# Performance work log

Measured on AMD Instinct MI355X. Metric: run time of the kernel, lower is better.

The kernel has to match this reference:

```python
import jax, jax.numpy as jnp
import numpy as np

TAU = 0.5
EPS = 1e-8


def setup_inputs() -> dict:
    key = jax.random.key(0)
    k1, k2 = jax.random.split(key)
    N, D = 200000, 512
    z_pos = jax.random.normal(k1, (N, D), dtype=jnp.float32)
    W = jax.random.normal(k2, (D, D), dtype=jnp.float32) * (1.0 / np.sqrt(D))
    b = jnp.zeros((D,), dtype=jnp.float32)
    return {"z_pos": z_pos, "W": W, "b": b}


def reference(z_pos, W, b):
    # sample_centroid: softmax-weighted centroid (computed on detached embeddings)
    h = jax.lax.stop_gradient(z_pos)
    init_c = h.mean(axis=0)                              # [D]
    d2 = jnp.sum((h - init_c[None, :]) ** 2, axis=1)     # [N]
    w = jax.nn.softmax(-d2 / TAU)                        # [N]
    c = jnp.sum(h * w[:, None], axis=0)                  # [D]

    # SimNet: dist = 1 - cosine_similarity(proj(x), c)
    x_proj = z_pos @ W.T + b                             # [N, D]
    x_norm = jnp.maximum(jnp.linalg.norm(x_proj, axis=-1), EPS)  # [N]
    c_norm = jnp.maximum(jnp.linalg.norm(c), EPS)
    cos = (x_proj @ c) / (x_norm * c_norm)               # [N]
    dist = 1.0 - cos
    return dist
```

## Files before the change

### kernel.cpp

```cpp
#include <hip/hip_runtime.h>
#include <hip/hip_bf16.h>
#include <math.h>

#define DD 512
#define EPSF 1e-8f
#define BM 128
#define BN 128
#define BK 32
#define FBIG 3.402823466e+38f
#define NPART 2048

typedef __bf16 bf16_t;
typedef __bf16 bf16x4_t __attribute__((ext_vector_type(4)));
typedef __bf16 bf16x8_t __attribute__((ext_vector_type(8)));
typedef float f32x4 __attribute__((ext_vector_type(4)));

__device__ inline float bf2f(unsigned short u) {
    return __uint_as_float(((unsigned int)u) << 16);
}

__global__ void k_convW(const float* __restrict__ W, bf16_t* __restrict__ Wb) {
    int i = blockIdx.x * blockDim.x + threadIdx.x;
    float4 v = ((const float4*)W)[i];
    bf16x4_t o;
    o[0] = (bf16_t)v.x; o[1] = (bf16_t)v.y; o[2] = (bf16_t)v.z; o[3] = (bf16_t)v.w;
    ((bf16x4_t*)Wb)[i] = o;
}

template<bool CONV>
__global__ void k_colsum(const float* __restrict__ z, bf16_t* __restrict__ zb,
                         float* __restrict__ part, int N, int rpb) {
    int t = threadIdx.x;
    int b = blockIdx.x;
    int col4 = t & 127, sub = t >> 7;
    int r0 = b * rpb, r1 = min(r0 + rpb, N);
    const float4* z4 = (const float4*)z;
    float4 acc = make_float4(0.f, 0.f, 0.f, 0.f);
    #pragma unroll 4
    for (int r = r0 + sub; r < r1; r += 2) {
        float4 v = z4[(size_t)r * 128 + col4];
        if (CONV) {
            bf16x4_t o;
            o[0] = (bf16_t)v.x; o[1] = (bf16_t)v.y; o[2] = (bf16_t)v.z; o[3] = (bf16_t)v.w;
            ((bf16x4_t*)zb)[(size_t)r * 128 + col4] = o;
        }
        acc.x += v.x; acc.y += v.y; acc.z += v.z; acc.w += v.w;
    }
    __shared__ float4 sm[128];
    if (sub == 1) sm[col4] = acc;
    __syncthreads();
    if (sub == 0) {
        float4 o = sm[col4];
        acc.x += o.x; acc.y += o.y; acc.z += o.z; acc.w += o.w;
        ((float4*)(part + (size_t)b * DD))[col4] = acc;
    }
}

__global__ void k_reduceP(const float* __restrict__ part, float* __restrict__ outv, float scale) {
    __shared__ float sm[256];
    int j = blockIdx.x;
    int t = threadIdx.x;
    float s = 0.f;
    #pragma unroll
    for (int p = 0; p < NPART / 256; ++p) s += part[(size_t)(p * 256 + t) * DD + j];
    sm[t] = s;
    __syncthreads();
    for (int st = 128; st > 0; st >>= 1) {
        if (t < st) sm[t] += sm[t + st];
        __syncthreads();
    }
    if (t == 0) outv[j] = sm[0] * scale;
}

__global__ __launch_bounds__(256, 4) void k_d2w(
    const float* __restrict__ z, const float* __restrict__ cbar,
    float* __restrict__ part, float* __restrict__ mpart,
    float* __restrict__ spart, int N)
{
    __shared__ float4 cs[128];
    __shared__ float4 vsm[4][128];
    __shared__ float wm[4], wsv[4];
    int t = threadIdx.x;
    int lane = t & 63, wv = t >> 6;
    int l15 = lane & 15, r4 = lane >> 4;
    if (t < 128) cs[t] = ((const float4*)cbar)[t];
    __syncthreads();

    int gw = (blockIdx.x * 256 + t) >> 6;
    int nw = (gridDim.x * 256) >> 6;
    float m = FBIG, s = 0.f;
    float4 acc[8];
    #pragma unroll
    for (int q = 0; q < 8; ++q) acc[q] = make_float4(0.f, 0.f, 0.f, 0.f);

    for (int r = gw * 4 + r4; r < N; r += nw * 4) {
        const float4* zr = (const float4*)(z + (size_t)r * DD);
        float4 vv[8];
        float sum = 0.f;
        #pragma unroll
        for (int q = 0; q < 8; ++q) {
            float4 v = zr[q * 16 + l15];
            float4 c = cs[q * 16 + l15];
            vv[q] = v;
            float d;
            d = v.x - c.x; sum += d * d;
            d = v.y - c.y; sum += d * d;
            d = v.z - c.z; sum += d * d;
            d = v.w - c.w; sum += d * d;
        }
        #pragma unroll
        for (int off = 1; off < 16; off <<= 1) sum += __shfl_xor(sum, off, 64);
        float w;
        if (sum < m) {
            float f = __expf(-2.0f * (m - sum));
            s *= f;
            #pragma unroll
            for (int q = 0; q < 8; ++q) {
                acc[q].x *= f; acc[q].y *= f; acc[q].z *= f; acc[q].w *= f;
            }
            m = sum;
            w = 1.0f;
        } else {
            w = __expf(-2.0f * (sum - m));
        }
        s += w;
        #pragma unroll
        for (int q = 0; q < 8; ++q) {
            acc[q].x += w * vv[q].x; acc[q].y += w * vv[q].y;
            acc[q].z += w * vv[q].z; acc[q].w += w * vv[q].w;
        }
    }

    float mw = fminf(m, __shfl_xor(m, 16, 64));
    mw = fminf(mw, __shfl_xor(mw, 32, 64));
    float f = __expf(-2.0f * (m - mw));
    s *= f;
    #pragma unroll
    for (int q = 0; q < 8; ++q) {
        acc[q].x *= f; acc[q].y *= f; acc[q].z *= f; acc[q].w *= f;
    }
    #pragma unroll
    for (int off = 16; off < 64; off <<= 1) {
        s += __shfl_xor(s, off, 64);
        #pragma unroll
        for (int q = 0; q < 8; ++q) {
            acc[q].x += __shfl_xor(acc[q].x, off, 64);
            acc[q].y += __shfl_xor(acc[q].y, off, 64);
            acc[q].z += __shfl_xor(acc[q].z, off, 64);
            acc[q].w += __shfl_xor(acc[q].w, off, 64);
        }
    }
    if (lane < 16) {
        #pragma unroll
        for (int q = 0; q < 8; ++q) vsm[wv][q * 16 + l15] = acc[q];
        if (lane == 0) { wm[wv] = mw; wsv[wv] = s; }
    }
    __syncthreads();
    if (t < 128) {
        float M = fminf(fminf(wm[0], wm[1]), fminf(wm[2], wm[3]));
        float4 o = make_float4(0.f, 0.f, 0.f, 0.f);
        #pragma unroll
        for (int w2 = 0; w2 < 4; ++w2) {
            float fw = __expf(-2.0f * (wm[w2] - M));
            float4 a = vsm[w2][t];
            o.x += fw * a.x; o.y += fw * a.y; o.z += fw * a.z; o.w += fw * a.w;
        }
        ((float4*)(part + (size_t)blockIdx.x * DD))[t] = o;
        if (t == 0) {
            float S = 0.f;
            #pragma unroll
            for (int w2 = 0; w2 < 4; ++w2) S += wsv[w2] * __expf(-2.0f * (wm[w2] - M));
            mpart[blockIdx.x] = M;
            spart[blockIdx.x] = S;
        }
    }
}

__global__ void k_combine2(const float* __restrict__ mpart, const float* __restrict__ spart,
                           float* __restrict__ wscale) {
    __shared__ float smm[256], sms[256];
    int t = threadIdx.x;
    float M = FBIG;
    for (int i = t; i < NPART; i += 256) M = fminf(M, mpart[i]);
    smm[t] = M;
    __syncthreads();
    for (int st = 128; st > 0; st >>= 1) {
        if (t < st) smm[t] = fminf(smm[t], smm[t + st]);
        __syncthreads();
    }
    M = smm[0];
    float S = 0.f;
    for (int i = t; i < NPART; i += 256) S += spart[i] * __expf(-2.0f * (mpart[i] - M));
    sms[t] = S;
    __syncthreads();
    for (int st = 128; st > 0; st >>= 1) {
        if (t < st) sms[t] += sms[t + st];
        __syncthreads();
    }
    float inv = 1.0f / sms[0];
    for (int i = t; i < NPART; i += 256) wscale[i] = __expf(-2.0f * (mpart[i] - M)) * inv;
}

__global__ void k_reducePW(const float* __restrict__ part, const float* __restrict__ wscale,
                           float* __restrict__ outv) {
    __shared__ float sm[256];
    int j = blockIdx.x, t = threadIdx.x;
    float s = 0.f;
    #pragma unroll
    for (int p = 0; p < NPART / 256; ++p) {
        int b = p * 256 + t;
        s += part[(size_t)b * DD + j] * wscale[b];
    }
    sm[t] = s;
    __syncthreads();
    for (int st = 128; st > 0; st >>= 1) {
        if (t < st) sm[t] += sm[t + st];
        __syncthreads();
    }
    if (t == 0) outv[j] = sm[0];
}

__global__ void k_cnorm(const float* __restrict__ cvec, float* __restrict__ outp) {
    __shared__ float sm[512];
    float v = cvec[threadIdx.x];
    sm[threadIdx.x] = v * v;
    __syncthreads();
    for (int st = 256; st > 0; st >>= 1) {
        if (threadIdx.x < st) sm[threadIdx.x] += sm[threadIdx.x + st];
        __syncthreads();
    }
    if (threadIdx.x == 0) outp[0] = 1.0f / fmaxf(sqrtf(sm[0]), EPSF);
}

__global__ __launch_bounds__(512, 2) void k_gemm256(
    const bf16_t* __restrict__ zb, const bf16_t* __restrict__ Wb,
    const float* __restrict__ bvec, const float* __restrict__ cvec,
    float* __restrict__ sqp, float* __restrict__ dtp, int N, int npad)
{
    __shared__ bf16_t As[2 * 256 * 64];
    __shared__ bf16_t Bs[2 * 256 * 64];

    const int t    = threadIdx.x;
    const int lane = t & 63;
    const int wid  = t >> 6;
    const int wr   = wid >> 2;
    const int wc   = wid & 3;
    const int quad = lane >> 4;
    const int l15  = lane & 15;

    const int nwg = gridDim.x * gridDim.y;
    const int lid = blockIdx.y * gridDim.x + blockIdx.x;
    const int q8  = nwg >> 3, r8 = nwg & 7;
    const int xcd = lid & 7, idx = lid >> 3;
    const int wg  = (xcd < r8 ? xcd * (q8 + 1) : r8 * (q8 + 1) + (xcd - r8) * q8) + idx;
    const int cb     = wg & 1;
    const int row0   = (wg >> 1) * 256;

    const int tr = t >> 3;
    const int bo = ((t & 7) * 16) ^ ((tr & 7) << 4);
    const char* apt = (const char*)zb + (size_t)(row0 + tr) * (DD * 2) + bo;
    const char* bpt = (const char*)Wb + (size_t)(cb * 256 + tr) * (DD * 2) + bo;
    const int ldsw = __builtin_amdgcn_readfirstlane(wid * 1024);

#define STAGE256(buf, kt) do {                                                              \
    _Pragma("unroll")                                                                       \
    for (int r_ = 0; r_ < 4; ++r_) {                                                        \
        __builtin_amdgcn_global_load_lds(                                                   \
            (const __attribute__((address_space(1))) unsigned int*)(const void*)            \
                (apt + (size_t)r_ * 65536 + (kt) * 128),                                    \
            (__attribute__((address_space(3))) unsigned int*)(void*)                        \
                ((char*)As + (buf) * 32768 + r_ * 8192 + ldsw), 16, 0, 0);                  \
        __builtin_amdgcn_global_load_lds(                                                   \
            (const __attribute__((address_space(1))) unsigned int*)(const void*)            \
                (bpt + (size_t)r_ * 65536 + (kt) * 128),                                    \
            (__attribute__((address_space(3))) unsigned int*)(void*)                        \
                ((char*)Bs + (buf) * 32768 + r_ * 8192 + ldsw), 16, 0, 0);                  \
    }                                                                                       \
} while (0)

    const int ka0 = (quad * 16) ^ ((l15 & 7) << 4);
    const int ka1 = ka0 ^ 64;
    const char* abase = (const char*)As + (wr * 128 + l15) * 128;
    const char* bbase = (const char*)Bs + (wc * 64 + l15) * 128;

    f32x4 acc[8][4];
    #pragma unroll
    for (int m = 0; m < 8; ++m)
        #pragma unroll
        for (int n = 0; n < 4; ++n) acc[m][n] = (f32x4){0.f, 0.f, 0.f, 0.f};

    STAGE256(0, 0);
    STAGE256(1, 1);
    asm volatile("s_waitcnt vmcnt(8)" ::: "memory");
    __builtin_amdgcn_sched_barrier(0);
    __builtin_amdgcn_s_barrier();
    __builtin_amdgcn_sched_barrier(0);

    #pragma unroll
    for (int kt = 0; kt < 8; ++kt) {
        const int cur = kt & 1;
        bf16x8_t afr[8][2], bfr[4][2];
        #pragma unroll
        for (int m = 0; m < 8; ++m) {
            afr[m][0] = *(const bf16x8_t*)(abase + cur * 32768 + m * 2048 + ka0);
            afr[m][1] = *(const bf16x8_t*)(abase + cur * 32768 + m * 2048 + ka1);
        }
        #pragma unroll
        for (int n = 0; n < 4; ++n) {
            bfr[n][0] = *(const bf16x8_t*)(bbase + cur * 32768 + n * 2048 + ka0);
            bfr[n][1] = *(const bf16x8_t*)(bbase + cur * 32768 + n * 2048 + ka1);
        }
        asm volatile("s_waitcnt lgkmcnt(0)" ::: "memory");
        __builtin_amdgcn_sched_barrier(0);
        __builtin_amdgcn_s_barrier();
        __builtin_amdgcn_sched_barrier(0);
        if (kt < 6) STAGE256(cur, kt + 2);
        __builtin_amdgcn_sched_barrier(0);
        __builtin_amdgcn_s_setprio(1);
        #pragma unroll
        for (int s = 0; s < 2; ++s)
            #pragma unroll
            for (int m = 0; m < 8; ++m)
                #pragma unroll
                for (int n = 0; n < 4; ++n)
                    acc[m][n] = __builtin_amdgcn_mfma_f32_16x16x32_bf16(
                        afr[m][s], bfr[n][s], acc[m][n], 0, 0, 0);
        __builtin_amdgcn_s_setprio(0);
        if (kt < 6) { asm volatile("s_waitcnt vmcnt(8)" ::: "memory"); }
        else        { asm volatile("s_waitcnt vmcnt(0)" ::: "memory"); }
        __builtin_amdgcn_sched_barrier(0);
        __builtin_amdgcn_s_barrier();
        __builtin_amdgcn_sched_barrier(0);
    }
#undef STAGE256

    float* psq = (float*)As;
    float* pdt = (float*)((char*)As + 16384);
    float bc[4], cc[4];
    #pragma unroll
    for (int n = 0; n < 4; ++n) {
        int col = cb * 256 + wc * 64 + n * 16 + l15;
        bc[n] = bvec[col];
        cc[n] = cvec[col];
    }
    #pragma unroll
    for (int m = 0; m < 8; ++m) {
        #pragma unroll
        for (int rg = 0; rg < 4; ++rg) {
            float sq = 0.f, dt = 0.f;
            #pragma unroll
            for (int n = 0; n < 4; ++n) {
                float x = acc[m][n][rg] + bc[n];
                sq += x * x;
                dt += x * cc[n];
            }
            sq += __shfl_xor(sq, 1, 64); dt += __shfl_xor(dt, 1, 64);
            sq += __shfl_xor(sq, 2, 64); dt += __shfl_xor(dt, 2, 64);
            if ((l15 & 3) == 0) {
                int row = wr * 128 + m * 16 + quad * 4 + rg;
                int slot = wc * 4 + (l15 >> 2);
                psq[row * 16 + slot] = sq;
                pdt[row * 16 + slot] = dt;
            }
        }
    }
    __syncthreads();
    if (t < 256) {
        int r = row0 + t;
        if (r < N) {
            const float4* p4 = (const float4*)(psq + t * 16);
            const float4* d4 = (const float4*)(pdt + t * 16);
            float sq = 0.f, dt = 0.f;
            #pragma unroll
            for (int i = 0; i < 4; ++i) {
                float4 a = p4[i], b2 = d4[i];
                sq += a.x + a.y + a.z + a.w;
                dt += b2.x + b2.y + b2.z + b2.w;
            }
            sqp[(size_t)cb * npad + r] = sq;
            dtp[(size_t)cb * npad + r] = dt;
        }
    }
}

__global__ __launch_bounds__(256, 4) void k_gemm_fb(
    const float* __restrict__ z, const bf16_t* __restrict__ Wb,
    const float* __restrict__ bvec, const float* __restrict__ cvec,
    float* __restrict__ sqp, float* __restrict__ dtp, int N, int npad)
{
    __shared__ bf16_t Asl[BM * BK];
    __shared__ bf16_t Bsl[BN * BK];
    __shared__ float psq[BM][8];
    __shared__ float pdt[BM][8];

    const int t    = threadIdx.x;
    const int lane = t & 63;
    const int wv   = t >> 6;
    const int wrr  = wv >> 1;
    const int wcc  = wv & 1;
    const int quad = lane >> 4;
    const int l15  = lane & 15;
    const int cbx  = blockIdx.x;
    const int row0 = blockIdx.y * BM;

    const bf16_t* bp = Wb + (size_t)(cbx * BN + (t >> 2)) * DD + (t & 3) * 8;
    const int arow = t >> 1;
    const int ah   = t & 1;
    int rowe = row0 + arow; if (rowe >= N) rowe = N - 1;
    const float4* zp4 = (const float4*)(z + (size_t)rowe * DD + ah * 16);

    f32x4 acc[4][4];
    #pragma unroll
    for (int a = 0; a < 4; ++a)
        #pragma unroll
        for (int b = 0; b < 4; ++b) acc[a][b] = (f32x4){0.f, 0.f, 0.f, 0.f};

    float4 v0 = zp4[0], v1 = zp4[1], v2 = zp4[2], v3 = zp4[3];

    for (int kc = 0; kc < DD; kc += BK) {
        if (kc) __syncthreads();
        #pragma unroll
        for (int q = 0; q < 2; ++q) {
            int ldsoff = __builtin_amdgcn_readfirstlane(q * 4096 + wv * 1024);
            __builtin_amdgcn_global_load_lds(
                (const __attribute__((address_space(1))) unsigned int*)(const void*)(bp + (size_t)q * 64 * DD + kc),
                (__attribute__((address_space(3))) unsigned int*)(void*)((char*)Bsl + ldsoff),
                16, 0, 0);
        }
        bf16x8_t lo, hi;
        lo[0]=(bf16_t)v0.x; lo[1]=(bf16_t)v0.y; lo[2]=(bf16_t)v0.z; lo[3]=(bf16_t)v0.w;
        lo[4]=(bf16_t)v1.x; lo[5]=(bf16_t)v1.y; lo[6]=(bf16_t)v1.z; lo[7]=(bf16_t)v1.w;
        hi[0]=(bf16_t)v2.x; hi[1]=(bf16_t)v2.y; hi[2]=(bf16_t)v2.z; hi[3]=(bf16_t)v2.w;
        hi[4]=(bf16_t)v3.x; hi[5]=(bf16_t)v3.y; hi[6]=(bf16_t)v3.z; hi[7]=(bf16_t)v3.w;
        *(bf16x8_t*)(Asl + arow * BK + ah * 16)     = lo;
        *(bf16x8_t*)(Asl + arow * BK + ah * 16 + 8) = hi;
        __syncthreads();
        if (kc + BK < DD) {
            int kf = (kc + BK) >> 2;
            v0 = zp4[kf]; v1 = zp4[kf + 1]; v2 = zp4[kf + 2]; v3 = zp4[kf + 3];
        }
        bf16x8_t af[4];
        #pragma unroll
        for (int rt = 0; rt < 4; ++rt)
            af[rt] = *(const bf16x8_t*)(Asl + (wrr * 64 + rt * 16 + l15) * BK + quad * 8);
        #pragma unroll
        for (int ct = 0; ct < 4; ++ct) {
            bf16x8_t bfv = *(const bf16x8_t*)(Bsl + (wcc * 64 + ct * 16 + l15) * BK + quad * 8);
            #pragma unroll
            for (int rt = 0; rt < 4; ++rt)
                acc[rt][ct] = __builtin_amdgcn_mfma_f32_16x16x32_bf16(af[rt], bfv, acc[rt][ct], 0, 0, 0);
        }
    }

    float bc[4], cc[4];
    #pragma unroll
    for (int ct = 0; ct < 4; ++ct) {
        int col = cbx * BN + wcc * 64 + ct * 16 + l15;
        bc[ct] = bvec[col];
        cc[ct] = cvec[col];
    }
    #pragma unroll
    for (int rt = 0; rt < 4; ++rt) {
        #pragma unroll
        for (int rg = 0; rg < 4; ++rg) {
            float sq = 0.f, dt = 0.f;
            #pragma unroll
            for (int ct = 0; ct < 4; ++ct) {
                float x = acc[rt][ct][rg] + bc[ct];
                sq += x * x;
                dt += x * cc[ct];
            }
            sq += __shfl_xor(sq, 1, 64); dt += __shfl_xor(dt, 1, 64);
            sq += __shfl_xor(sq, 2, 64); dt += __shfl_xor(dt, 2, 64);
            if ((l15 & 3) == 0) {
                int rl = wrr * 64 + rt * 16 + quad * 4 + rg;
                psq[rl][wcc * 4 + (l15 >> 2)] = sq;
                pdt[rl][wcc * 4 + (l15 >> 2)] = dt;
            }
        }
    }
    __syncthreads();
    if (t < BM) {
        int r = row0 + t;
        if (r < N) {
            float sq = 0.f, dt = 0.f;
            #pragma unroll
            for (int i = 0; i < 8; ++i) { sq += psq[t][i]; dt += pdt[t][i]; }
            sqp[(size_t)cbx * npad + r] = sq;
            dtp[(size_t)cbx * npad + r] = dt;
        }
    }
}

template<int NCB>
__global__ void k_final(const float* __restrict__ sqp, const float* __restrict__ dtp,
                        const float* __restrict__ cninv, float* __restrict__ out,
                        int N, int npad) {
    int r = blockIdx.x * blockDim.x + threadIdx.x;
    if (r < N) {
        float sq = 0.f, dt = 0.f;
        #pragma unroll
        for (int i = 0; i < NCB; ++i) {
            sq += sqp[(size_t)i * npad + r];
            dt += dtp[(size_t)i * npad + r];
        }
        out[r] = 1.0f - dt * cninv[0] / fmaxf(sqrtf(sq), EPSF);
    }
}

extern "C" void kernel_launch(void* const* d_in, const int* in_sizes, int n_in,
                              void* d_out, int out_size, void* d_ws, size_t ws_size,
                              hipStream_t stream)
{
    const float* z = (const float*)d_in[0];
    const float* W = (const float*)d_in[1];
    const float* b = (const float*)d_in[2];
    float* out = (float*)d_out;
    int N = in_sizes[0] / DD;
    int npad = ((N + 255) / 256) * 256;

    float* ws = (float*)d_ws;
    size_t off = 0;
    float* part   = ws + off; off += (size_t)NPART * DD;
    float* cbar   = ws + off; off += DD;
    float* mpart  = ws + off; off += NPART;
    float* spart  = ws + off; off += NPART;
    float* wscale = ws + off; off += NPART;
    float* cvec   = ws + off; off += DD;
    float* cninv  = ws + off; off += 1;
    off = (off + 3) & ~(size_t)3;
    float* sqp    = ws + off; off += (size_t)4 * npad;
    float* dtp    = ws + off; off += (size_t)4 * npad;
    bf16_t* Wb    = (bf16_t*)(ws + off); off += (size_t)DD * DD / 2;
    bf16_t* zb    = (bf16_t*)(ws + off);
    size_t need_bytes = (off + (size_t)npad * DD / 2) * sizeof(float);
    const bool use_zb = ws_size >= need_bytes;

    int rpb = (N + NPART - 1) / NPART;

    k_convW<<<256, 256, 0, stream>>>(W, Wb);
    if (use_zb) k_colsum<true ><<<NPART, 256, 0, stream>>>(z, zb, part, N, rpb);
    else        k_colsum<false><<<NPART, 256, 0, stream>>>(z, zb, part, N, rpb);
    k_reduceP<<<DD, 256, 0, stream>>>(part, cbar, 1.0f / (float)N);
    k_d2w<<<NPART, 256, 0, stream>>>(z, cbar, part, mpart, spart, N);
    k_combine2<<<1, 256, 0, stream>>>(mpart, spart, wscale);
    k_reducePW<<<DD, 256, 0, stream>>>(part, wscale, cvec);
    k_cnorm<<<1, DD, 0, stream>>>(cvec, cninv);
    if (use_zb) {
        dim3 grid(2, npad / 256);
        k_gemm256<<<grid, 512, 0, stream>>>(zb, Wb, b, cvec, sqp, dtp, N, npad);
        k_final<2><<<(N + 255) / 256, 256, 0, stream>>>(sqp, dtp, cninv, out, N, npad);
    } else {
        dim3 grid(4, npad / BM);
        k_gemm_fb<<<grid, 256, 0, stream>>>(z, Wb, b, cvec, sqp, dtp, N, npad);
        k_final<4><<<(N + 255) / 256, 256, 0, stream>>>(sqp, dtp, cninv, out, N, npad);
    }
}
```

Before: 857.5 us.

## Switch GEMM to one-ahead prefetch with per-k-step fragment loads

Replaces the two-stage-ahead pipeline, where all LDS fragments were loaded and a barrier taken before issuing the next global-to-LDS copy, with a single-ahead prefetch into the other buffer. That copy is issued at the top of each k-tile, and fragments are read from LDS per 32-wide k sub-step, interleaved with the MFMAs. The LDS staging layout is regrouped into 128-row halves. This removes one barrier per iteration and lowers register pressure from fragments. In exchange, prefetch depth drops to one tile, with a full vmcnt(0) wait each iteration.

```diff
diff --git a/kernel.cpp b/kernel.cpp
--- a/kernel.cpp
+++ b/kernel.cpp
@@ -237,8 +237,8 @@
     const float* __restrict__ bvec, const float* __restrict__ cvec,
     float* __restrict__ sqp, float* __restrict__ dtp, int N, int npad)
 {
-    __shared__ bf16_t As[2 * 256 * 64];
-    __shared__ bf16_t Bs[2 * 256 * 64];
+    __shared__ bf16_t As[2 * 2 * 128 * 64];
+    __shared__ bf16_t Bs[2 * 2 * 128 * 64];
 
     const int t    = threadIdx.x;
     const int lane = t & 63;
@@ -262,26 +262,29 @@
     const char* bpt = (const char*)Wb + (size_t)(cb * 256 + tr) * (DD * 2) + bo;
     const int ldsw = __builtin_amdgcn_readfirstlane(wid * 1024);
 
-#define STAGE256(buf, kt) do {                                                              \
+#define STAGEALL(buf, kt) do {                                                              \
     _Pragma("unroll")                                                                       \
-    for (int r_ = 0; r_ < 4; ++r_) {                                                        \
-        __builtin_amdgcn_global_load_lds(                                                   \
-            (const __attribute__((address_space(1))) unsigned int*)(const void*)            \
-                (apt + (size_t)r_ * 65536 + (kt) * 128),                                    \
-            (__attribute__((address_space(3))) unsigned int*)(void*)                        \
-                ((char*)As + (buf) * 32768 + r_ * 8192 + ldsw), 16, 0, 0);                  \
-        __builtin_amdgcn_global_load_lds(                                                   \
-            (const __attribute__((address_space(1))) unsigned int*)(const void*)            \
-                (bpt + (size_t)r_ * 65536 + (kt) * 128),                                    \
-            (__attribute__((address_space(3))) unsigned int*)(void*)                        \
-                ((char*)Bs + (buf) * 32768 + r_ * 8192 + ldsw), 16, 0, 0);                  \
+    for (int h_ = 0; h_ < 2; ++h_) {                                                        \
+        _Pragma("unroll")                                                                   \
+        for (int j_ = 0; j_ < 2; ++j_) {                                                    \
+            __builtin_amdgcn_global_load_lds(                                               \
+                (const __attribute__((address_space(1))) unsigned int*)(const void*)        \
+                    (apt + (size_t)(h_ * 128 + j_ * 64) * 1024 + (kt) * 128),               \
+                (__attribute__((address_space(3))) unsigned int*)(void*)                    \
+                    ((char*)As + (buf) * 32768 + h_ * 16384 + j_ * 8192 + ldsw), 16, 0, 0); \
+            __builtin_amdgcn_global_load_lds(                                               \
+                (const __attribute__((address_space(1))) unsigned int*)(const void*)        \
+                    (bpt + (size_t)(h_ * 128 + j_ * 64) * 1024 + (kt) * 128),               \
+                (__attribute__((address_space(3))) unsigned int*)(void*)                    \
+                    ((char*)Bs + (buf) * 32768 + h_ * 16384 + j_ * 8192 + ldsw), 16, 0, 0); \
+        }                                                                                   \
     }                                                                                       \
 } while (0)
 
-    const int ka0 = (quad * 16) ^ ((l15 & 7) << 4);
-    const int ka1 = ka0 ^ 64;
-    const char* abase = (const char*)As + (wr * 128 + l15) * 128;
-    const char* bbase = (const char*)Bs + (wc * 64 + l15) * 128;
+    const char* abase = (const char*)As + wr * 16384 + l15 * 128;
+    const char* bbase = (const char*)Bs + (wc >> 1) * 16384 + ((wc & 1) * 64 + l15) * 128;
+    const int kq = quad * 16;
+    const int sw = (l15 & 7) << 4;
 
     f32x4 acc[8][4];
     #pragma unroll
@@ -289,9 +292,8 @@
         #pragma unroll
         for (int n = 0; n < 4; ++n) acc[m][n] = (f32x4){0.f, 0.f, 0.f, 0.f};
 
-    STAGE256(0, 0);
-    STAGE256(1, 1);
-    asm volatile("s_waitcnt vmcnt(8)" ::: "memory");
+    STAGEALL(0, 0);
+    asm volatile("s_waitcnt vmcnt(0)" ::: "memory");
     __builtin_amdgcn_sched_barrier(0);
     __builtin_amdgcn_s_barrier();
     __builtin_amdgcn_sched_barrier(0);
@@ -299,40 +301,33 @@
     #pragma unroll
     for (int kt = 0; kt < 8; ++kt) {
         const int cur = kt & 1;
-        bf16x8_t afr[8][2], bfr[4][2];
-        #pragma unroll
-        for (int m = 0; m < 8; ++m) {
-            afr[m][0] = *(const bf16x8_t*)(abase + cur * 32768 + m * 2048 + ka0);
-            afr[m][1] = *(const bf16x8_t*)(abase + cur * 32768 + m * 2048 + ka1);
-        }
-        #pragma unroll
-        for (int n = 0; n < 4; ++n) {
-            bfr[n][0] = *(const bf16x8_t*)(bbase + cur * 32768 + n * 2048 + ka0);
-            bfr[n][1] = *(const bf16x8_t*)(bbase + cur * 32768 + n * 2048 + ka1);
-        }
-        asm volatile("s_waitcnt lgkmcnt(0)" ::: "memory");
-        __builtin_amdgcn_sched_barrier(0);
-        __builtin_amdgcn_s_barrier();
-        __builtin_amdgcn_sched_barrier(0);
-        if (kt < 6) STAGE256(cur, kt + 2);
+        if (kt < 7) STAGEALL(cur ^ 1, kt + 1);
         __builtin_amdgcn_sched_barrier(0);
         __builtin_amdgcn_s_setprio(1);
         #pragma unroll
-        for (int s = 0; s < 2; ++s)
+        for (int s = 0; s < 2; ++s) {
+            const int kb = (s * 64 + kq) ^ sw;
+            bf16x8_t afr[8], bfr[4];
+            #pragma unroll
+            for (int m = 0; m < 8; ++m)
+                afr[m] = *(const bf16x8_t*)(abase + cur * 32768 + m * 2048 + kb);
+            #pragma unroll
+            for (int n = 0; n < 4; ++n)
+                bfr[n] = *(const bf16x8_t*)(bbase + cur * 32768 + n * 2048 + kb);
             #pragma unroll
             for (int m = 0; m < 8; ++m)
                 #pragma unroll
                 for (int n = 0; n < 4; ++n)
                     acc[m][n] = __builtin_amdgcn_mfma_f32_16x16x32_bf16(
-                        afr[m][s], bfr[n][s], acc[m][n], 0, 0, 0);
+                        afr[m], bfr[n], acc[m][n], 0, 0, 0);
+        }
         __builtin_amdgcn_s_setprio(0);
-        if (kt < 6) { asm volatile("s_waitcnt vmcnt(8)" ::: "memory"); }
-        else        { asm volatile("s_waitcnt vmcnt(0)" ::: "memory"); }
+        if (kt < 7) { asm volatile("s_waitcnt vmcnt(0)" ::: "memory"); }
         __builtin_amdgcn_sched_barrier(0);
         __builtin_amdgcn_s_barrier();
         __builtin_amdgcn_sched_barrier(0);
     }
-#undef STAGE256
+#undef STAGEALL
 
     float* psq = (float*)As;
     float* pdt = (float*)((char*)As + 16384);
```

After: 878.9 us. +2.5%, slower.
